# Optimization experiments

Hardware: AMD Instinct MI355X
Metric: run time of the kernel (lower is better)

The kernel has to match this reference:

```python
import jax, jax.numpy as jnp
import numpy as np

N_NODES = 50000
N_EDGES = 800000
D_IN = 128
D_OUT = 128
K = 3


def setup_inputs() -> dict:
    key = jax.random.key(0)
    k1, k2, k3, k4 = jax.random.split(key, 4)
    x = jax.random.normal(k1, (N_NODES, D_IN), dtype=jnp.float32)
    W = jax.random.normal(k2, (K, D_IN, D_OUT), dtype=jnp.float32) * 0.05
    edge_index = jax.random.randint(k3, (K, 2, N_EDGES), 0, N_NODES, dtype=jnp.int32)
    edge_weight = jax.random.uniform(k4, (K, N_EDGES), dtype=jnp.float32)
    return {"x": x, "W": W, "edge_index": edge_index, "edge_weight": edge_weight}


def reference(x, W, edge_index, edge_weight):
    # ChebConv: out = sum_k A_k @ (x @ W_k), A_k given as weighted edge lists.
    n = x.shape[0]
    out = jnp.zeros((n, W.shape[-1]), dtype=x.dtype)
    for k in range(W.shape[0]):
        h = x @ W[k]                                   # [N, D_OUT] dense GEMM
        src = edge_index[k, 0]
        dst = edge_index[k, 1]
        msg = h[src] * edge_weight[k][:, None]         # [E, D_OUT] gather + scale
        out = out + jax.ops.segment_sum(msg, dst, num_segments=n)
    return out
```

## Files before the change

### kernel.cpp

```cpp
#include <hip/hip_runtime.h>
#include <hip/hip_bf16.h>

#define N_NODES 50000
#define N_EDGES 800000
#define D 128
#define KCHEB 3
#define NBKT 98
#define TOTB (KCHEB * NBKT)
#define SLAB 16384
#define EPB 2048
#define NBLK_E ((N_EDGES + EPB - 1) / EPB)

typedef __attribute__((ext_vector_type(8))) short short8v;
typedef __attribute__((ext_vector_type(4))) float f32x4;

__device__ inline unsigned f2bf(float f) {
    unsigned x = __float_as_uint(f);
    unsigned r = ((x >> 16) & 1u) + 0x7FFFu;
    return (x + r) >> 16;
}

__global__ __launch_bounds__(256) void wprep(const float* __restrict__ W,
                                             unsigned short* __restrict__ Wtg) {
    const int k = blockIdx.x;
    const float* Wk = W + (size_t)k * D * D;
    unsigned short* o = Wtg + (size_t)k * D * D;
    for (int i = threadIdx.x; i < 4096; i += 256) {
        int r  = i >> 5;
        int c4 = (i & 31) * 4;
        float4 wv = *(const float4*)&Wk[r * 128 + c4];
        #pragma unroll
        for (int j = 0; j < 4; ++j) {
            int row = c4 + j;
            int byte_in_row = (r * 2) ^ ((row & 7) << 4);
            o[row * 128 + (byte_in_row >> 1)] = (unsigned short)f2bf((&wv.x)[j]);
        }
    }
}

__global__ __launch_bounds__(256) void gemm_mfma(const float* __restrict__ x,
                                                 const unsigned short* __restrict__ Wtg,
                                                 unsigned* __restrict__ h3, int n) {
    __shared__ unsigned short Wt[128 * 128];
    const int t = threadIdx.x;
    unsigned* h2 = h3 + (size_t)blockIdx.y * N_NODES * 64;

    {
        const uint4* src = (const uint4*)(Wtg + (size_t)blockIdx.y * D * D);
        uint4* dst = (uint4*)Wt;
        #pragma unroll
        for (int i = 0; i < 8; ++i) dst[t + 256 * i] = src[t + 256 * i];
    }
    __syncthreads();

    const int lane = t & 63, w = t >> 6;
    const int m0 = blockIdx.x * 64 + w * 16;
    const int arow = m0 + (lane & 15);
    const float* xr = x + (size_t)(arow < n ? arow : 0) * D + ((lane >> 4) << 3);

    short8v afr[4];
    #pragma unroll
    for (int kt = 0; kt < 4; ++kt) {
        float4 p0 = *(const float4*)(xr + kt * 32);
        float4 p1 = *(const float4*)(xr + kt * 32 + 4);
        union { short8v s; unsigned u[4]; } a;
        a.u[0] = f2bf(p0.x) | (f2bf(p0.y) << 16);
        a.u[1] = f2bf(p0.z) | (f2bf(p0.w) << 16);
        a.u[2] = f2bf(p1.x) | (f2bf(p1.y) << 16);
        a.u[3] = f2bf(p1.z) | (f2bf(p1.w) << 16);
        afr[kt] = a.s;
    }

    f32x4 acc[8] = {};
    const int kb = (lane >> 4) << 4;
    #pragma unroll
    for (int nn = 0; nn < 8; ++nn) {
        const int row = nn * 16 + (lane & 15);
        const int sw = (row & 7) << 4;
        const unsigned short* wr = &Wt[row * 128];
        #pragma unroll
        for (int kt = 0; kt < 4; ++kt) {
            int byte_in_row = ((kt << 6) + kb) ^ sw;
            short8v b = *(const short8v*)&wr[byte_in_row >> 1];
            acc[nn] = __builtin_amdgcn_mfma_f32_16x16x32_bf16(afr[kt], b, acc[nn], 0, 0, 0);
        }
    }

    unsigned short* hs = (unsigned short*)h2;
    const int orow_base = m0 + ((lane >> 4) << 2);
    const int col_base = lane & 15;
    #pragma unroll
    for (int nn = 0; nn < 8; ++nn) {
        int col = nn * 16 + col_base;
        #pragma unroll
        for (int r = 0; r < 4; ++r) {
            int orow = orow_base + r;
            if (orow < n) hs[(size_t)orow * D + col] = (unsigned short)f2bf(acc[nn][r]);
        }
    }
}

__global__ __launch_bounds__(256) void bucket_bin(const int* __restrict__ ei,
                                                  const float* __restrict__ ew,
                                                  int* __restrict__ cursor,
                                                  uint2* __restrict__ binned) {
    __shared__ int lh[NBKT], gb[NBKT], lc[NBKT];
    const int k = blockIdx.y, t = threadIdx.x;
    for (int i = t; i < NBKT; i += 256) { lh[i] = 0; lc[i] = 0; }
    __syncthreads();
    const int* srcs = ei + (size_t)k * 2 * N_EDGES;
    const int* dsts = srcs + N_EDGES;
    const float* w = ew + (size_t)k * N_EDGES;
    const int base = blockIdx.x * EPB;
    #pragma unroll
    for (int q = 0; q < EPB / 1024; ++q) {
        int e = base + q * 1024 + t * 4;
        if (e < N_EDGES) {
            int4 d4 = *(const int4*)&dsts[e];
            atomicAdd(&lh[d4.x >> 9], 1);
            atomicAdd(&lh[d4.y >> 9], 1);
            atomicAdd(&lh[d4.z >> 9], 1);
            atomicAdd(&lh[d4.w >> 9], 1);
        }
    }
    __syncthreads();
    for (int i = t; i < NBKT; i += 256)
        gb[i] = lh[i] ? atomicAdd(&cursor[k * NBKT + i], lh[i]) : 0;
    __syncthreads();
    #pragma unroll
    for (int q = 0; q < EPB / 1024; ++q) {
        int e = base + q * 1024 + t * 4;
        if (e < N_EDGES) {
            int4 d4 = *(const int4*)&dsts[e];
            int4 s4 = *(const int4*)&srcs[e];
            float4 w4 = *(const float4*)&w[e];
            #pragma unroll
            for (int j = 0; j < 4; ++j) {
                int d = (&d4.x)[j];
                int b = d >> 9;
                int pos = (k * NBKT + b) * SLAB + gb[b] + atomicAdd(&lc[b], 1);
                binned[pos] = make_uint2(__float_as_uint((&w4.x)[j]),
                                         (unsigned)(&s4.x)[j] | ((unsigned)(d & 511) << 16));
            }
        }
    }
}

__global__ __launch_bounds__(256) void build_csr(const uint2* __restrict__ binned,
                                                 const int* __restrict__ cursor,
                                                 int* __restrict__ off,
                                                 int* __restrict__ num,
                                                 unsigned* __restrict__ csr4) {
    __shared__ int nh[512], ex[512], wsum[4];
    const int kb = blockIdx.x;
    const int k = kb / NBKT, b = kb % NBKT;
    const int t = threadIdx.x;
    const int beg = kb * SLAB;
    const int end = beg + cursor[kb];

    for (int i = t; i < 512; i += 256) nh[i] = 0;
    __syncthreads();
    for (int i = beg + t; i < end; i += 256)
        atomicAdd(&nh[(binned[i].y >> 16) & 511], 1);
    __syncthreads();

    int a0 = nh[2 * t], a1 = nh[2 * t + 1];
    int s = a0 + a1;
    int lane = t & 63, wid = t >> 6;
    int v = s;
    #pragma unroll
    for (int d = 1; d < 64; d <<= 1) {
        int u = __shfl_up(v, d, 64);
        if (lane >= d) v += u;
    }
    if (lane == 63) wsum[wid] = v;
    __syncthreads();
    int wb = 0;
    for (int i = 0; i < wid; ++i) wb += wsum[i];
    int ep = wb + v - s;
    ex[2 * t] = ep;
    ex[2 * t + 1] = ep + a0;

    const int node0 = b * 512;
    int n0 = node0 + 2 * t, n1 = node0 + 2 * t + 1;
    if (n0 < N_NODES) { off[k * N_NODES + n0] = beg + ep;      num[k * N_NODES + n0] = a0; }
    if (n1 < N_NODES) { off[k * N_NODES + n1] = beg + ep + a0; num[k * N_NODES + n1] = a1; }

    for (int i = t; i < 512; i += 256) nh[i] = 0;
    __syncthreads();
    for (int i = beg + t; i < end; i += 256) {
        uint2 e = binned[i];
        int dl = (e.y >> 16) & 511;
        int pos = beg + ex[dl] + atomicAdd(&nh[dl], 1);
        csr4[pos] = (e.y & 0xFFFFu) | (f2bf(__uint_as_float(e.x)) << 16);
    }
}

__global__ __launch_bounds__(256) void gather_all(const unsigned* __restrict__ h3,
                                                  const unsigned* __restrict__ csr4,
                                                  const int* __restrict__ off,
                                                  const int* __restrict__ num,
                                                  float* __restrict__ out) {
    const int half = threadIdx.x >> 5;
    const int l = threadIdx.x & 31;
    const int node = blockIdx.x * 8 + half;
    if (node >= N_NODES) return;

    float a0 = 0.f, a1 = 0.f, a2 = 0.f, a3 = 0.f;
    #pragma unroll
    for (int k = 0; k < KCHEB; ++k) {
        const unsigned* h2 = h3 + (size_t)k * N_NODES * 64;
        const int kd = k * N_NODES + node;
        int i = off[kd];
        const int end = i + num[kd];
        for (; i + 8 <= end; i += 8) {
            unsigned e[8];
            uint2 u[8];
            #pragma unroll
            for (int j = 0; j < 8; ++j) e[j] = csr4[i + j];
            #pragma unroll
            for (int j = 0; j < 8; ++j)
                u[j] = *(const uint2*)&h2[(size_t)(e[j] & 0xFFFFu) * 64 + l * 2];
            #pragma unroll
            for (int j = 0; j < 8; ++j) {
                float w = __uint_as_float(e[j] & 0xFFFF0000u);
                a0 += w * __uint_as_float(u[j].x << 16);
                a1 += w * __uint_as_float(u[j].x & 0xFFFF0000u);
                a2 += w * __uint_as_float(u[j].y << 16);
                a3 += w * __uint_as_float(u[j].y & 0xFFFF0000u);
            }
        }
        for (; i < end; ++i) {
            unsigned e = csr4[i];
            float w = __uint_as_float(e & 0xFFFF0000u);
            uint2 u = *(const uint2*)&h2[(size_t)(e & 0xFFFFu) * 64 + l * 2];
            a0 += w * __uint_as_float(u.x << 16);
            a1 += w * __uint_as_float(u.x & 0xFFFF0000u);
            a2 += w * __uint_as_float(u.y << 16);
            a3 += w * __uint_as_float(u.y & 0xFFFF0000u);
        }
    }
    *(float4*)&out[(size_t)node * D + l * 4] = make_float4(a0, a1, a2, a3);
}

extern "C" void kernel_launch(void* const* d_in, const int* in_sizes, int n_in,
                              void* d_out, int out_size, void* d_ws, size_t ws_size,
                              hipStream_t stream) {
    const float* x  = (const float*)d_in[0];
    const float* W  = (const float*)d_in[1];
    const int*   ei = (const int*)d_in[2];
    const float* ew = (const float*)d_in[3];
    float* out = (float*)d_out;

    char* ws = (char*)d_ws;
    unsigned*       csr4   = (unsigned*)      (ws);
    uint2*          binned = (uint2*)         (ws + 19267584);
    unsigned*       h3     = (unsigned*)      (ws + 57802752);
    int*            off    = (int*)           (ws + 96202752);
    int*            num    = (int*)           (ws + 96802752);
    int*            cursor = (int*)           (ws + 97402752);
    unsigned short* Wtg    = (unsigned short*)(ws + 97403936);

    hipMemsetAsync(cursor, 0, TOTB * sizeof(int), stream);

    wprep<<<KCHEB, 256, 0, stream>>>(W, Wtg);

    const dim3 egrid(NBLK_E, KCHEB);
    bucket_bin<<<egrid, 256, 0, stream>>>(ei, ew, cursor, binned);

    const dim3 ggrid((N_NODES + 63) / 64, KCHEB);
    gemm_mfma<<<ggrid, 256, 0, stream>>>(x, Wtg, h3, N_NODES);

    build_csr<<<TOTB, 256, 0, stream>>>(binned, cursor, off, num, csr4);

    const int gat_grid = (N_NODES + 7) / 8;
    gather_all<<<gat_grid, 256, 0, stream>>>(h3, csr4, off, num, out);
}
```

Baseline: 264.5 us.

## Reuse x fragments across Chebyshev orders, split binned arrays, widen gather loads

The GEMM kernel now loops over all three weight matrices inside one block, so x is loaded and converted to bf16 once instead of three times. The binned edge record is split into a 4-byte meta array and a 2-byte bf16 weight array, which cuts intermediate write and read traffic in bucket_bin and build_csr. The gather kernel uses 16 lanes per node with 16-byte loads of h, giving fewer but wider gather transactions. The trade-offs are less GEMM parallelism (one third as many blocks) and more registers per gather thread.

```diff
diff --git a/kernel.cpp b/kernel.cpp
--- a/kernel.cpp
+++ b/kernel.cpp
@@ -43,16 +43,6 @@
                                                  unsigned* __restrict__ h3, int n) {
     __shared__ unsigned short Wt[128 * 128];
     const int t = threadIdx.x;
-    unsigned* h2 = h3 + (size_t)blockIdx.y * N_NODES * 64;
-
-    {
-        const uint4* src = (const uint4*)(Wtg + (size_t)blockIdx.y * D * D);
-        uint4* dst = (uint4*)Wt;
-        #pragma unroll
-        for (int i = 0; i < 8; ++i) dst[t + 256 * i] = src[t + 256 * i];
-    }
-    __syncthreads();
-
     const int lane = t & 63, w = t >> 6;
     const int m0 = blockIdx.x * 64 + w * 16;
     const int arow = m0 + (lane & 15);
@@ -71,31 +61,43 @@
         afr[kt] = a.s;
     }
 
-    f32x4 acc[8] = {};
     const int kb = (lane >> 4) << 4;
-    #pragma unroll
-    for (int nn = 0; nn < 8; ++nn) {
-        const int row = nn * 16 + (lane & 15);
-        const int sw = (row & 7) << 4;
-        const unsigned short* wr = &Wt[row * 128];
-        #pragma unroll
-        for (int kt = 0; kt < 4; ++kt) {
-            int byte_in_row = ((kt << 6) + kb) ^ sw;
-            short8v b = *(const short8v*)&wr[byte_in_row >> 1];
-            acc[nn] = __builtin_amdgcn_mfma_f32_16x16x32_bf16(afr[kt], b, acc[nn], 0, 0, 0);
-        }
-    }
-
-    unsigned short* hs = (unsigned short*)h2;
     const int orow_base = m0 + ((lane >> 4) << 2);
     const int col_base = lane & 15;
-    #pragma unroll
-    for (int nn = 0; nn < 8; ++nn) {
-        int col = nn * 16 + col_base;
+
+    for (int kc = 0; kc < KCHEB; ++kc) {
+        __syncthreads();
+        {
+            const uint4* src = (const uint4*)(Wtg + (size_t)kc * D * D);
+            uint4* dst = (uint4*)Wt;
+            #pragma unroll
+            for (int i = 0; i < 8; ++i) dst[t + 256 * i] = src[t + 256 * i];
+        }
+        __syncthreads();
+
+        f32x4 acc[8] = {};
         #pragma unroll
-        for (int r = 0; r < 4; ++r) {
-            int orow = orow_base + r;
-            if (orow < n) hs[(size_t)orow * D + col] = (unsigned short)f2bf(acc[nn][r]);
+        for (int nn = 0; nn < 8; ++nn) {
+            const int row = nn * 16 + (lane & 15);
+            const int sw = (row & 7) << 4;
+            const unsigned short* wr = &Wt[row * 128];
+            #pragma unroll
+            for (int kt = 0; kt < 4; ++kt) {
+                int byte_in_row = ((kt << 6) + kb) ^ sw;
+                short8v b = *(const short8v*)&wr[byte_in_row >> 1];
+                acc[nn] = __builtin_amdgcn_mfma_f32_16x16x32_bf16(afr[kt], b, acc[nn], 0, 0, 0);
+            }
+        }
+
+        unsigned short* hs = (unsigned short*)(h3 + (size_t)kc * N_NODES * 64);
+        #pragma unroll
+        for (int nn = 0; nn < 8; ++nn) {
+            int col = nn * 16 + col_base;
+            #pragma unroll
+            for (int r = 0; r < 4; ++r) {
+                int orow = orow_base + r;
+                if (orow < n) hs[(size_t)orow * D + col] = (unsigned short)f2bf(acc[nn][r]);
+            }
         }
     }
 }
@@ -103,7 +105,8 @@
 __global__ __launch_bounds__(256) void bucket_bin(const int* __restrict__ ei,
                                                   const float* __restrict__ ew,
                                                   int* __restrict__ cursor,
-                                                  uint2* __restrict__ binned) {
+                                                  unsigned* __restrict__ bmeta,
+                                                  unsigned short* __restrict__ bw) {
     __shared__ int lh[NBKT], gb[NBKT], lc[NBKT];
     const int k = blockIdx.y, t = threadIdx.x;
     for (int i = t; i < NBKT; i += 256) { lh[i] = 0; lc[i] = 0; }
@@ -139,14 +142,15 @@
                 int d = (&d4.x)[j];
                 int b = d >> 9;
                 int pos = (k * NBKT + b) * SLAB + gb[b] + atomicAdd(&lc[b], 1);
-                binned[pos] = make_uint2(__float_as_uint((&w4.x)[j]),
-                                         (unsigned)(&s4.x)[j] | ((unsigned)(d & 511) << 16));
-            }
-        }
-    }
-}
-
-__global__ __launch_bounds__(256) void build_csr(const uint2* __restrict__ binned,
+                bmeta[pos] = (unsigned)(&s4.x)[j] | ((unsigned)(d & 511) << 16);
+                bw[pos] = (unsigned short)f2bf((&w4.x)[j]);
+            }
+        }
+    }
+}
+
+__global__ __launch_bounds__(256) void build_csr(const unsigned* __restrict__ bmeta,
+                                                 const unsigned short* __restrict__ bw,
                                                  const int* __restrict__ cursor,
                                                  int* __restrict__ off,
                                                  int* __restrict__ num,
@@ -161,7 +165,7 @@
     for (int i = t; i < 512; i += 256) nh[i] = 0;
     __syncthreads();
     for (int i = beg + t; i < end; i += 256)
-        atomicAdd(&nh[(binned[i].y >> 16) & 511], 1);
+        atomicAdd(&nh[(bmeta[i] >> 16) & 511], 1);
     __syncthreads();
 
     int a0 = nh[2 * t], a1 = nh[2 * t + 1];
@@ -189,10 +193,10 @@
     for (int i = t; i < 512; i += 256) nh[i] = 0;
     __syncthreads();
     for (int i = beg + t; i < end; i += 256) {
-        uint2 e = binned[i];
-        int dl = (e.y >> 16) & 511;
+        unsigned m = bmeta[i];
+        int dl = (m >> 16) & 511;
         int pos = beg + ex[dl] + atomicAdd(&nh[dl], 1);
-        csr4[pos] = (e.y & 0xFFFFu) | (f2bf(__uint_as_float(e.x)) << 16);
+        csr4[pos] = (m & 0xFFFFu) | ((unsigned)bw[i] << 16);
     }
 }
 
@@ -201,12 +205,13 @@
                                                   const int* __restrict__ off,
                                                   const int* __restrict__ num,
                                                   float* __restrict__ out) {
-    const int half = threadIdx.x >> 5;
-    const int l = threadIdx.x & 31;
-    const int node = blockIdx.x * 8 + half;
+    const int q = threadIdx.x >> 4;
+    const int l = threadIdx.x & 15;
+    const int node = blockIdx.x * 16 + q;
     if (node >= N_NODES) return;
 
     float a0 = 0.f, a1 = 0.f, a2 = 0.f, a3 = 0.f;
+    float a4 = 0.f, a5 = 0.f, a6 = 0.f, a7 = 0.f;
     #pragma unroll
     for (int k = 0; k < KCHEB; ++k) {
         const unsigned* h2 = h3 + (size_t)k * N_NODES * 64;
@@ -215,12 +220,12 @@
         const int end = i + num[kd];
         for (; i + 8 <= end; i += 8) {
             unsigned e[8];
-            uint2 u[8];
+            uint4 u[8];
             #pragma unroll
             for (int j = 0; j < 8; ++j) e[j] = csr4[i + j];
             #pragma unroll
             for (int j = 0; j < 8; ++j)
-                u[j] = *(const uint2*)&h2[(size_t)(e[j] & 0xFFFFu) * 64 + l * 2];
+                u[j] = *(const uint4*)&h2[(size_t)(e[j] & 0xFFFFu) * 64 + l * 4];
             #pragma unroll
             for (int j = 0; j < 8; ++j) {
                 float w = __uint_as_float(e[j] & 0xFFFF0000u);
@@ -228,19 +233,29 @@
                 a1 += w * __uint_as_float(u[j].x & 0xFFFF0000u);
                 a2 += w * __uint_as_float(u[j].y << 16);
                 a3 += w * __uint_as_float(u[j].y & 0xFFFF0000u);
+                a4 += w * __uint_as_float(u[j].z << 16);
+                a5 += w * __uint_as_float(u[j].z & 0xFFFF0000u);
+                a6 += w * __uint_as_float(u[j].w << 16);
+                a7 += w * __uint_as_float(u[j].w & 0xFFFF0000u);
             }
         }
         for (; i < end; ++i) {
             unsigned e = csr4[i];
             float w = __uint_as_float(e & 0xFFFF0000u);
-            uint2 u = *(const uint2*)&h2[(size_t)(e & 0xFFFFu) * 64 + l * 2];
+            uint4 u = *(const uint4*)&h2[(size_t)(e & 0xFFFFu) * 64 + l * 4];
             a0 += w * __uint_as_float(u.x << 16);
             a1 += w * __uint_as_float(u.x & 0xFFFF0000u);
             a2 += w * __uint_as_float(u.y << 16);
             a3 += w * __uint_as_float(u.y & 0xFFFF0000u);
-        }
-    }
-    *(float4*)&out[(size_t)node * D + l * 4] = make_float4(a0, a1, a2, a3);
+            a4 += w * __uint_as_float(u.z << 16);
+            a5 += w * __uint_as_float(u.z & 0xFFFF0000u);
+            a6 += w * __uint_as_float(u.w << 16);
+            a7 += w * __uint_as_float(u.w & 0xFFFF0000u);
+        }
+    }
+    float* op = &out[(size_t)node * D + l * 8];
+    *(float4*)(op)     = make_float4(a0, a1, a2, a3);
+    *(float4*)(op + 4) = make_float4(a4, a5, a6, a7);
 }
 
 extern "C" void kernel_launch(void* const* d_in, const int* in_sizes, int n_in,
@@ -254,25 +269,25 @@
 
     char* ws = (char*)d_ws;
     unsigned*       csr4   = (unsigned*)      (ws);
-    uint2*          binned = (uint2*)         (ws + 19267584);
-    unsigned*       h3     = (unsigned*)      (ws + 57802752);
-    int*            off    = (int*)           (ws + 96202752);
-    int*            num    = (int*)           (ws + 96802752);
-    int*            cursor = (int*)           (ws + 97402752);
-    unsigned short* Wtg    = (unsigned short*)(ws + 97403936);
+    unsigned*       bmeta  = (unsigned*)      (ws + 19267584);
+    unsigned short* bw     = (unsigned short*)(ws + 38535168);
+    unsigned*       h3     = (unsigned*)      (ws + 48168960);
+    int*            off    = (int*)           (ws + 86568960);
+    int*            num    = (int*)           (ws + 87168960);
+    int*            cursor = (int*)           (ws + 87768960);
+    unsigned short* Wtg    = (unsigned short*)(ws + 87770136);
 
     hipMemsetAsync(cursor, 0, TOTB * sizeof(int), stream);
 
     wprep<<<KCHEB, 256, 0, stream>>>(W, Wtg);
 
     const dim3 egrid(NBLK_E, KCHEB);
-    bucket_bin<<<egrid, 256, 0, stream>>>(ei, ew, cursor, binned);
-
-    const dim3 ggrid((N_NODES + 63) / 64, KCHEB);
-    gemm_mfma<<<ggrid, 256, 0, stream>>>(x, Wtg, h3, N_NODES);
-
-    build_csr<<<TOTB, 256, 0, stream>>>(binned, cursor, off, num, csr4);
-
-    const int gat_grid = (N_NODES + 7) / 8;
+    bucket_bin<<<egrid, 256, 0, stream>>>(ei, ew, cursor, bmeta, bw);
+
+    gemm_mfma<<<(N_NODES + 63) / 64, 256, 0, stream>>>(x, Wtg, h3, N_NODES);
+
+    build_csr<<<TOTB, 256, 0, stream>>>(bmeta, bw, cursor, off, num, csr4);
+
+    const int gat_grid = (N_NODES + 15) / 16;
     gather_all<<<gat_grid, 256, 0, stream>>>(h3, csr4, off, num, out);
 }
```

Result: slower. 280.3 us (+6.0%).
